# Optimization experiments

Measured on AMD Instinct MI355X. Metric: run time of the kernel, lower is better.

The kernel has to match this reference:

```python
import jax, jax.numpy as jnp
import numpy as np

L = 5          # number of pyramid levels (cat_fuse expects 5*C input channels)
C = 192        # in_channels, divisible by 3 and 2
C3 = C // 3
C2 = C // 2
B = 4
SIZES = [(192, 192), (96, 96), (48, 48), (24, 24), (12, 12)]  # x[1] is reference scale


def conv1x1(x, w, b):
    # 1x1 conv (+ folded eval-mode BN): x [n,cin,h,w], w [cout,cin], b [cout]
    return jnp.einsum('oc,nchw->nohw', w, x) + b[None, :, None, None]


def setup_inputs() -> dict:
    key = jax.random.key(0)
    ks = iter(jax.random.split(key, 40))
    inp = {}
    for i, (h, w) in enumerate(SIZES):
        inp[f'x{i}'] = jax.random.normal(next(ks), (B, C, h, w), jnp.float32)
    def wp(shape):
        return jax.random.normal(next(ks), shape, jnp.float32) * 0.05
    for nm, co, ci in [('k1', C3, C), ('k2', C3, C), ('k3', C3, C), ('q', C, C), ('v', C, C),
                       ('cf', C, L * C), ('e1', C2, C), ('e2', C, C2), ('r1', C2, C), ('r2', C, C2)]:
        inp['W_' + nm] = wp((co, ci))
        inp['b_' + nm] = wp((co,))
    inp['bn_s'] = 1.0 + wp((C,))   # standalone BN folded to affine scale
    inp['bn_t'] = wp((C,))         # standalone BN folded to affine shift
    return inp


def reference(x0, x1, x2, x3, x4,
              W_k1, b_k1, W_k2, b_k2, W_k3, b_k3,
              W_q, b_q, W_v, b_v, W_cf, b_cf,
              W_e1, b_e1, W_e2, b_e2, W_r1, b_r1, W_r2, b_r2,
              bn_s, bn_t):
    xs = [x0, x1, x2, x3, x4]
    b, _, h, w = x1.shape
    hw = h * w
    # bilinear resize to reference scale (torch F.interpolate align_corners=False)
    x_up = [x1 if i == 1 else jax.image.resize(x, (b, C, h, w), 'bilinear') for i, x in enumerate(xs)]
    Xf = jnp.stack(x_up).reshape(L * b, C, h, w)  # shared weights across levels -> batch them

    def emb(z):  # conv1x1 -> GELU(exact) -> conv1x1 (dropout is identity at eval)
        return conv1x1(jax.nn.gelu(conv1x1(z, W_e1, b_e1), approximate=False), W_e2, b_e2)

    la_res = None
    for k in range(5):
        # residual refinement: relu(bn(x + res_block(x)))
        r = conv1x1(jax.nn.relu(conv1x1(Xf, W_r1, b_r1)), W_r2, b_r2)
        Xf = jax.nn.relu((Xf + r) * bn_s[None, :, None, None] + bn_t[None, :, None, None])
        # query/value: per-level projection, split C into 3 chunks -> 15 'keys' per pixel
        Q = conv1x1(Xf, W_q, b_q).reshape(L, b, 3, C3, hw)
        Q = Q.transpose(1, 0, 2, 3, 4).reshape(b, 3 * L, C3, hw).transpose(0, 3, 2, 1)  # [b,hw,C3,15]
        V = conv1x1(Xf, W_v, b_v).reshape(L, b, 3, C3, hw)
        V = V.transpose(1, 0, 2, 3, 4).reshape(b, 3 * L, C3, hw).transpose(0, 3, 1, 2)  # [b,hw,15,C3]
        if k == 0:
            cat = Xf.reshape(L, b, C, h, w).transpose(1, 0, 2, 3, 4).reshape(b, L * C, h, w)
            la_res = emb(jax.nn.relu(conv1x1(cat, W_cf, b_cf)))
        refs = []
        for Wk, bk in ((W_k1, b_k1), (W_k2, b_k2), (W_k3, b_k3)):
            key_i = conv1x1(la_res, Wk, bk).reshape(b, C3, hw).transpose(0, 2, 1)       # [b,hw,C3]
            att = jax.nn.softmax(jnp.einsum('bpc,bpck->bpk', key_i, Q), axis=-1)        # [b,hw,15]
            ref = jnp.einsum('bpk,bpkc->bpc', att, V)                                   # [b,hw,C3]
            refs.append(ref.transpose(0, 2, 1).reshape(b, C3, h, w))
        la_res = emb(jnp.concatenate(refs, axis=1))
    return la_res
```

## Files before the change

### kernel.cpp

```cpp
#include <hip/hip_runtime.h>
#include <math.h>

typedef unsigned short u16;
typedef unsigned int   u32;
typedef __bf16 bf16x8 __attribute__((ext_vector_type(8)));
typedef float  f32x4  __attribute__((ext_vector_type(4)));

__device__ __forceinline__ float b2f(u16 u) {
    unsigned v = ((unsigned)u) << 16;
    return __uint_as_float(v);
}
__device__ __forceinline__ u16 f2b(float f) {
    unsigned x = __float_as_uint(f);
    unsigned r = (x + 0x7fffu + ((x >> 16) & 1u)) >> 16;
    return (u16)r;
}
__device__ __forceinline__ void fsplit(float v, u16& h, u16& l) {
    h = f2b(v);
    l = f2b(v - b2f(h));
}
__device__ __forceinline__ float h2f(u16 u) {
    union { u16 us; _Float16 h; } c; c.us = u; return (float)c.h;
}
__device__ __forceinline__ u16 f2h(float f) {
    union { u16 us; _Float16 h; } c; c.h = (_Float16)f; return c.us;
}
__device__ __forceinline__ float ldx(const void* p, size_t i, int f32m) {
    return f32m ? ((const float*)p)[i] : b2f(((const u16*)p)[i]);
}

__device__ __forceinline__ void gld16(u16* l, const u16* g) {
    __builtin_amdgcn_global_load_lds(
        (const __attribute__((address_space(1))) unsigned int*)g,
        (__attribute__((address_space(3))) unsigned int*)l,
        16, 0, 0);
}

__device__ __forceinline__ int swz(int row) {
    return (row & 3) ^ ((row >> 2) & 3);
}

__global__ void detect_dtype(const u16* __restrict__ x0, int* flag)
{
    int lane = threadIdx.x;
    int bad = 0;
    for (int i = lane; i < 1024; i += 64) {
        float v = b2f(x0[i]);
        if (!(fabsf(v) < 32768.f)) bad = 1;
    }
    unsigned long long m = __ballot(bad);
    if (lane == 0) flag[0] = (m != 0ULL) ? 1 : 0;
}

struct SrcPtrs {
    const void *wr1, *br1, *wr2, *br2, *wq, *bq, *wv, *bv, *wcf, *bcf;
    const void *we1, *be1, *we2, *be2, *wk1, *bk1, *wk2, *bk2, *wk3, *bk3;
    const void *bns, *bnt;
};
__global__ void pack_weights(SrcPtrs S, u16* __restrict__ Wh, u16* __restrict__ Wl,
                             float* __restrict__ Bias, const int* __restrict__ dflag)
{
    const int f32m = *dflag;
    int idx = blockIdx.x * 256 + threadIdx.x;
    if (idx < 368640) {
        const void* src; size_t si;
        if (idx < 18432)       { src = S.wr1; si = idx; }
        else if (idx < 36864)  { src = S.wr2; si = idx - 18432; }
        else if (idx < 110592) {
            int r = idx - 36864, o = r / 192, c = r % 192;
            if (o < 192) { src = S.wq; si = (size_t)o * 192 + c; }
            else         { src = S.wv; si = (size_t)(o - 192) * 192 + c; }
        }
        else if (idx < 294912) { src = S.wcf; si = idx - 110592; }
        else if (idx < 313344) { src = S.we1; si = idx - 294912; }
        else if (idx < 331776) { src = S.we2; si = idx - 313344; }
        else {
            int r = idx - 331776, o = r / 192, c = r % 192;
            src = (o < 64) ? S.wk1 : ((o < 128) ? S.wk2 : S.wk3);
            si = (size_t)(o & 63) * 192 + c;
        }
        u16 h, l; fsplit(ldx(src, si, f32m), h, l);
        Wh[idx] = h; Wl[idx] = l;
    } else if (idx < 370368) {
        int b = idx - 368640; const void* src; size_t si;
        if (b < 96)        { src = S.br1; si = b; }
        else if (b < 288)  { src = S.br2; si = b - 96; }
        else if (b < 672)  { int r = b - 288;
                             if (r < 192) { src = S.bq; si = r; }
                             else         { src = S.bv; si = r - 192; } }
        else if (b < 864)  { src = S.bcf; si = b - 672; }
        else if (b < 960)  { src = S.be1; si = b - 864; }
        else if (b < 1152) { src = S.be2; si = b - 960; }
        else if (b < 1344) { int r = b - 1152;
                             src = (r < 64) ? S.bk1 : ((r < 128) ? S.bk2 : S.bk3);
                             si = r & 63; }
        else if (b < 1536) { src = S.bns; si = b - 1344; }
        else               { src = S.bnt; si = b - 1536; }
        Bias[b] = ldx(src, si, f32m);
    }
}

__global__ void build_tables(float* __restrict__ wtab, int* __restrict__ jtab)
{
    int t = threadIdx.x;
    if (t >= 384) return;
    int li = t / 96, o = t % 96;
    const int ins[4] = {192, 48, 24, 12};
    int in = ins[li];
    float scale = (float)in / 96.0f;
    float ksc = fmaxf(scale, 1.0f);
    float cc = (o + 0.5f) * scale - 0.5f;
    float w[4] = {0.f, 0.f, 0.f, 0.f};
    int   j[4] = {0, 0, 0, 0};
    int n = 0; float s = 0.f;
    int jl = (int)floorf(cc - ksc), jh = (int)floorf(cc + ksc) + 1;
    for (int jj = jl; jj <= jh; jj++) {
        if (jj < 0 || jj >= in) continue;
        float ww = 1.0f - fabsf((float)jj - cc) / ksc;
        if (ww <= 0.f) continue;
        if (n < 4) { w[n] = ww; j[n] = jj; s += ww; n++; }
    }
    for (int i = 0; i < 4; i++) {
        wtab[li * 384 + o * 4 + i] = w[i] / s;
        jtab[li * 384 + o * 4 + i] = j[i];
    }
}

template<int SPLIT>
__launch_bounds__(256)
__global__ void transpose_in(const void* __restrict__ src, int HW,
                             u32* __restrict__ P, u16* __restrict__ Xh,
                             u16* __restrict__ Xl, const int* __restrict__ dflag)
{
    __shared__ float t[32][33];
    const int f32m = *dflag;
    const int b  = blockIdx.z;
    const int c0 = blockIdx.y * 32;
    const int p0 = blockIdx.x * 32;
    const int tid = threadIdx.x;
#pragma unroll
    for (int it = 0; it < 4; it++) {
        int i = it * 256 + tid;
        int pl = i & 31, cl = i >> 5;
        int p = p0 + pl;
        float v = 0.f;
        if (p < HW) v = ldx(src, ((size_t)(b * 192 + c0 + cl)) * HW + p, f32m);
        t[pl][cl] = v;
    }
    __syncthreads();
#pragma unroll
    for (int it = 0; it < 4; it++) {
        int i = it * 256 + tid;
        int cl = i & 31, pl = i >> 5;
        int p = p0 + pl;
        if (p >= HW) continue;
        float v = t[pl][cl];
        u16 h, l; fsplit(v, h, l);
        if constexpr (SPLIT) {
            size_t oi = ((size_t)((4 + b) * 9216 + p)) * 192 + c0 + cl;
            Xh[oi] = h; Xl[oi] = l;
        } else {
            P[((size_t)b * HW + p) * 192 + c0 + cl] = (u32)h | ((u32)l << 16);
        }
    }
}

template<int TAPS>
__launch_bounds__(256)
__global__ void upsample2(const u32* __restrict__ Pa, const u32* __restrict__ Pb,
                          const u32* __restrict__ Pc,
                          const float* __restrict__ wtab, const int* __restrict__ jtab,
                          u16* __restrict__ Xh, u16* __restrict__ Xl)
{
    int li, b, l, in;
    const u32* P;
    if constexpr (TAPS == 4) {
        li = 0; b = blockIdx.y; l = 0; in = 192; P = Pa;
    } else {
        int yi = blockIdx.y;
        li = 1 + (yi >> 2); b = yi & 3;
        const int lvl[4] = {0, 2, 3, 4};
        const int ins[4] = {192, 48, 24, 12};
        l = lvl[li]; in = ins[li];
        P = (li == 1) ? Pa : ((li == 2) ? Pb : Pc);
    }
    int gid = blockIdx.x * 256 + threadIdx.x;
    int c = gid % 192;
    int p = gid / 192;
    int y = p / 96, x = p % 96;
    const float* wt = wtab + li * 384;
    const int*   jt = jtab + li * 384;

    size_t ib = (size_t)b * in * in * 192 + c;
    float a = 0.f;
#pragma unroll
    for (int iy = 0; iy < TAPS; iy++) {
        float wy = wt[y * 4 + iy];
        size_t rb = ib + (size_t)(jt[y * 4 + iy] * in) * 192;
        float ax = 0.f;
#pragma unroll
        for (int ix = 0; ix < TAPS; ix++) {
            u32 u = P[rb + jt[x * 4 + ix] * 192];
            ax += wt[x * 4 + ix] * (b2f((u16)u) + b2f((u16)(u >> 16)));
        }
        a += wy * ax;
    }
    size_t oi = ((size_t)(l * 4 + b) * 9216 + p) * 192 + c;
    u16 h, lo; fsplit(a, h, lo);
    Xh[oi] = h; Xl[oi] = lo;
}

template<int NT, int ACT, int MODE, int OUT>
__launch_bounds__(256)
__global__ void conv_gemm(const u16* __restrict__ Ah, const u16* __restrict__ Al,
                          const u16* __restrict__ Wh, const u16* __restrict__ Wl,
                          const float* __restrict__ Bias,
                          int woff, int boff, int K, int O,
                          u16* __restrict__ out0, u16* __restrict__ out1)
{
    __shared__ __align__(16) u16 LDS[32768];

    const int tid  = threadIdx.x;
    const int lane = tid & 63, wave = tid >> 6;
    const int qd   = lane >> 4, ln = lane & 15;
    const int p0   = blockIdx.x * 64;
    const int img  = blockIdx.z;
    const int M    = 9216;
    const int irow = tid >> 2, ich = tid & 3;

    auto issue = [&](int kb, int c) {
        u16* S = LDS + c * 16384;
        {
            int ch = ich ^ swz(irow);
            size_t ga;
            if constexpr (MODE == 2) {
                int l = kb / 192;
                ga = ((size_t)((l * 4 + img) * M + p0 + irow)) * 192 + (kb - l * 192) + ch * 8;
            } else {
                ga = ((size_t)(img * M + p0 + irow)) * (size_t)K + kb + ch * 8;
            }
            gld16(S + wave * 512,        Ah + ga);
            gld16(S + 2048 + wave * 512, Al + ga);
        }
#pragma unroll
        for (int i = 0; i < 3; i++) {
            int idx = i * 256 + tid;
            int brow = idx >> 2;
            int bc = (idx & 3) ^ swz(brow);
            size_t gb = (size_t)woff + (size_t)brow * K + kb + bc * 8;
            gld16(S + 4096 + i * 2048 + wave * 512,  Wh + gb);
            gld16(S + 10240 + i * 2048 + wave * 512, Wl + gb);
        }
    };

    f32x4 acc[NT];
#pragma unroll
    for (int j = 0; j < NT; j++) acc[j] = (f32x4){0.f, 0.f, 0.f, 0.f};

    issue(0, 0);
    __syncthreads();
    for (int kb = 0; kb < K; kb += 32) {
        int cur = (kb >> 5) & 1;
        if (kb + 32 < K) issue(kb + 32, cur ^ 1);
        const u16* S = LDS + cur * 16384;
        int arow = wave * 16 + ln;
        int asl = arow * 32 + ((qd ^ swz(arow)) << 3);
        bf16x8 ah = *(const bf16x8*)&S[asl];
        bf16x8 al = *(const bf16x8*)&S[2048 + asl];
#pragma unroll
        for (int j = 0; j < NT; j++) {
            int brow = j * 16 + ln;
            int bsl = brow * 32 + ((qd ^ swz(brow)) << 3);
            bf16x8 bh = *(const bf16x8*)&S[4096 + bsl];
            bf16x8 bl = *(const bf16x8*)&S[10240 + bsl];
            acc[j] = __builtin_amdgcn_mfma_f32_16x16x32_bf16(ah, bh, acc[j], 0, 0, 0);
            acc[j] = __builtin_amdgcn_mfma_f32_16x16x32_bf16(ah, bl, acc[j], 0, 0, 0);
            acc[j] = __builtin_amdgcn_mfma_f32_16x16x32_bf16(al, bh, acc[j], 0, 0, 0);
        }
        __syncthreads();
    }

#pragma unroll
    for (int j = 0; j < NT; j++) {
        int o = j * 16 + ln;
        float bvf = Bias[boff + o];
#pragma unroll
        for (int r = 0; r < 4; r++) {
            int prow = p0 + wave * 16 + qd * 4 + r;
            float v = acc[j][r] + bvf;
            if constexpr (ACT == 1) v = fmaxf(v, 0.f);
            if constexpr (OUT == 0) {
                size_t oidx = ((size_t)(img * M + prow)) * (size_t)O + o;
                u16 h, l; fsplit(v, h, l);
                out0[oidx] = h; out1[oidx] = l;
            } else if constexpr (OUT == 1) {
                out0[((size_t)(img * M + prow)) * (size_t)O + o] = f2h(v);
            } else {
                size_t pb = ((size_t)(img * M + prow)) * 192;
                if (o < 192) out0[pb + o] = f2h(v);
                else         out1[pb + o - 192] = f2h(v);
            }
        }
    }
}

template<int ACT1, int MODE2>
__launch_bounds__(256)
__global__ void fused_mlp(const u16* __restrict__ Ah, const u16* __restrict__ Al,
                          const u16* __restrict__ Wh, const u16* __restrict__ Wl,
                          const float* __restrict__ Bias,
                          int w1off, int b1off, int w2off, int b2off,
                          u16* __restrict__ outh, u16* __restrict__ outl)
{
    __shared__ __align__(16) u16 LDS[38912];
    u16* Hh = LDS;
    u16* Hl = LDS + 6656;

    const int tid  = threadIdx.x;
    const int lane = tid & 63, wave = tid >> 6;
    const int qd   = lane >> 4, ln = lane & 15;
    const int p0   = blockIdx.x * 64;
    const int img  = blockIdx.z;
    const int M    = 9216;
    const int irow = tid >> 2, ich = tid & 3;

    auto g1issue = [&](int kb, int c) {
        u16* SA = LDS + 13312 + c * 10240;
        int ch = ich ^ swz(irow);
        size_t ga = ((size_t)(img * M + p0 + irow)) * 192 + kb + ch * 8;
        gld16(SA + wave * 512,        Ah + ga);
        gld16(SA + 2048 + wave * 512, Al + ga);
        size_t gb = (size_t)w1off + (size_t)irow * 192 + kb + ch * 8;
        gld16(SA + 4096 + wave * 512, Wh + gb);
        gld16(SA + 7168 + wave * 512, Wl + gb);
        if (tid < 128) {
            int r2 = 64 + irow;
            int ch2 = ich ^ swz(r2);
            size_t gb2 = (size_t)w1off + (size_t)r2 * 192 + kb + ch2 * 8;
            gld16(SA + 6144 + wave * 512, Wh + gb2);
            gld16(SA + 9216 + wave * 512, Wl + gb2);
        }
    };
    auto g2issue = [&](int kb, int c) {
        u16* B2 = LDS + 13312 + c * 12288;
#pragma unroll
        for (int i = 0; i < 3; i++) {
            int r = i * 64 + irow;
            int ch = ich ^ swz(r);
            size_t g = (size_t)w2off + (size_t)r * 96 + kb + ch * 8;
            gld16(B2 + i * 2048 + wave * 512,        Wh + g);
            gld16(B2 + 6144 + i * 2048 + wave * 512, Wl + g);
        }
    };

    f32x4 acc1[6];
#pragma unroll
    for (int j = 0; j < 6; j++) acc1[j] = (f32x4){0.f, 0.f, 0.f, 0.f};

    g1issue(0, 0);
    __syncthreads();
#pragma unroll 2
    for (int kb = 0; kb < 192; kb += 32) {
        int cur = (kb >> 5) & 1;
        if (kb + 32 < 192) g1issue(kb + 32, cur ^ 1);
        const u16* SA = LDS + 13312 + cur * 10240;
        int arow = wave * 16 + ln;
        int asl = arow * 32 + ((qd ^ swz(arow)) << 3);
        bf16x8 ah = *(const bf16x8*)&SA[asl];
        bf16x8 al = *(const bf16x8*)&SA[2048 + asl];
#pragma unroll
        for (int j = 0; j < 6; j++) {
            int brow = j * 16 + ln;
            int bsl = brow * 32 + ((qd ^ swz(brow)) << 3);
            bf16x8 bh = *(const bf16x8*)&SA[4096 + bsl];
            bf16x8 bl = *(const bf16x8*)&SA[7168 + bsl];
            acc1[j] = __builtin_amdgcn_mfma_f32_16x16x32_bf16(ah, bh, acc1[j], 0, 0, 0);
            acc1[j] = __builtin_amdgcn_mfma_f32_16x16x32_bf16(ah, bl, acc1[j], 0, 0, 0);
            acc1[j] = __builtin_amdgcn_mfma_f32_16x16x32_bf16(al, bh, acc1[j], 0, 0, 0);
        }
        __syncthreads();
    }

    g2issue(0, 0);
#pragma unroll
    for (int j = 0; j < 6; j++) {
        int o = j * 16 + ln;
        float bvf = Bias[b1off + o];
#pragma unroll
        for (int r = 0; r < 4; r++) {
            float v = acc1[j][r] + bvf;
            if constexpr (ACT1 == 1) v = fmaxf(v, 0.f);
            if constexpr (ACT1 == 2) v = 0.5f * v * (1.f + erff(v * 0.70710678118654752f));
            u16 h, l; fsplit(v, h, l);
            int row = wave * 16 + qd * 4 + r;
            Hh[row * 104 + o] = h;
            Hl[row * 104 + o] = l;
        }
    }
    __syncthreads();

    f32x4 acc2[12];
#pragma unroll
    for (int j = 0; j < 12; j++) acc2[j] = (f32x4){0.f, 0.f, 0.f, 0.f};

#pragma unroll
    for (int kb = 0; kb < 96; kb += 32) {
        int cur = (kb >> 5) & 1;
        if (kb + 32 < 96) g2issue(kb + 32, cur ^ 1);
        const u16* B2 = LDS + 13312 + cur * 12288;
        bf16x8 ah = *(const bf16x8*)&Hh[(wave * 16 + ln) * 104 + kb + qd * 8];
        bf16x8 al = *(const bf16x8*)&Hl[(wave * 16 + ln) * 104 + kb + qd * 8];
#pragma unroll
        for (int j = 0; j < 12; j++) {
            int brow = j * 16 + ln;
            int bsl = brow * 32 + ((qd ^ swz(brow)) << 3);
            bf16x8 bh = *(const bf16x8*)&B2[bsl];
            bf16x8 bl = *(const bf16x8*)&B2[6144 + bsl];
            acc2[j] = __builtin_amdgcn_mfma_f32_16x16x32_bf16(ah, bh, acc2[j], 0, 0, 0);
            acc2[j] = __builtin_amdgcn_mfma_f32_16x16x32_bf16(ah, bl, acc2[j], 0, 0, 0);
            acc2[j] = __builtin_amdgcn_mfma_f32_16x16x32_bf16(al, bh, acc2[j], 0, 0, 0);
        }
        __syncthreads();
    }

#pragma unroll
    for (int j = 0; j < 12; j++) {
        int o = j * 16 + ln;
        float bvf = Bias[b2off + o];
#pragma unroll
        for (int r = 0; r < 4; r++) {
            int prow = p0 + wave * 16 + qd * 4 + r;
            float v = acc2[j][r] + bvf;
            size_t oidx = ((size_t)(img * M + prow)) * 192 + o;
            if constexpr (MODE2 == 1) {
                float xo = b2f(outh[oidx]) + b2f(outl[oidx]);
                v = fmaxf((xo + v) * Bias[1344 + o] + Bias[1536 + o], 0.f);
            }
            u16 h, l; fsplit(v, h, l);
            outh[oidx] = h; outl[oidx] = l;
        }
    }
}

template<int WRITE_X>
__launch_bounds__(256)
__global__ void fused_res_qv(u16* __restrict__ Xh, u16* __restrict__ Xl,
                             const u16* __restrict__ Wh, const u16* __restrict__ Wl,
                             const float* __restrict__ Bias,
                             u16* __restrict__ Qf, u16* __restrict__ Vf)
{
    __shared__ __align__(16) u16 LDS[38912];
    u16* Hh = LDS;
    u16* Hl = LDS + 6656;

    const int tid  = threadIdx.x;
    const int lane = tid & 63, wave = tid >> 6;
    const int qd   = lane >> 4, ln = lane & 15;
    const int p0   = blockIdx.x * 64;
    const int img  = blockIdx.z;
    const int M    = 9216;
    const int irow = tid >> 2, ich = tid & 3;

    auto g1issue = [&](int kb, int c) {
        u16* SA = LDS + 13312 + c * 10240;
        int ch = ich ^ swz(irow);
        size_t ga = ((size_t)(img * M + p0 + irow)) * 192 + kb + ch * 8;
        gld16(SA + wave * 512,        Xh + ga);
        gld16(SA + 2048 + wave * 512, Xl + ga);
        size_t gb = (size_t)irow * 192 + kb + ch * 8;
        gld16(SA + 4096 + wave * 512, Wh + gb);
        gld16(SA + 7168 + wave * 512, Wl + gb);
        if (tid < 128) {
            int r2 = 64 + irow;
            int ch2 = ich ^ swz(r2);
            size_t gb2 = (size_t)r2 * 192 + kb + ch2 * 8;
            gld16(SA + 6144 + wave * 512, Wh + gb2);
            gld16(SA + 9216 + wave * 512, Wl + gb2);
        }
    };
    auto g2issue = [&](int kb, int c) {
        u16* B2 = LDS + 13312 + c * 12288;
#pragma unroll
        for (int i = 0; i < 3; i++) {
            int r = i * 64 + irow;
            int ch = ich ^ swz(r);
            size_t g = (size_t)18432 + (size_t)r * 96 + kb + ch * 8;
            gld16(B2 + i * 2048 + wave * 512,        Wh + g);
            gld16(B2 + 6144 + i * 2048 + wave * 512, Wl + g);
        }
    };
    auto g3issue = [&](int s, int c) {
        int p = s / 6, kb = (s - p * 6) * 32;
        u16* B3 = LDS + 24576 + c * 6144;
        int ch = ich ^ swz(irow);
        size_t g = (size_t)36864 + (size_t)(p * 96 + irow) * 192 + kb + ch * 8;
        gld16(B3 + wave * 512,        Wh + g);
        gld16(B3 + 3072 + wave * 512, Wl + g);
        if (tid < 128) {
            int r2 = 64 + irow;
            int ch2 = ich ^ swz(r2);
            size_t g2 = (size_t)36864 + (size_t)(p * 96 + r2) * 192 + kb + ch2 * 8;
            gld16(B3 + 2048 + wave * 512, Wh + g2);
            gld16(B3 + 5120 + wave * 512, Wl + g2);
        }
    };

    f32x4 acc1[6];
#pragma unroll
    for (int j = 0; j < 6; j++) acc1[j] = (f32x4){0.f, 0.f, 0.f, 0.f};

    g1issue(0, 0);
    __syncthreads();
#pragma unroll 2
    for (int kb = 0; kb < 192; kb += 32) {
        int cur = (kb >> 5) & 1;
        if (kb + 32 < 192) g1issue(kb + 32, cur ^ 1);
        const u16* SA = LDS + 13312 + cur * 10240;
        int arow = wave * 16 + ln;
        int asl = arow * 32 + ((qd ^ swz(arow)) << 3);
        bf16x8 ah = *(const bf16x8*)&SA[asl];
        bf16x8 al = *(const bf16x8*)&SA[2048 + asl];
#pragma unroll
        for (int j = 0; j < 6; j++) {
            int brow = j * 16 + ln;
            int bsl = brow * 32 + ((qd ^ swz(brow)) << 3);
            bf16x8 bh = *(const bf16x8*)&SA[4096 + bsl];
            bf16x8 bl = *(const bf16x8*)&SA[7168 + bsl];
            acc1[j] = __builtin_amdgcn_mfma_f32_16x16x32_bf16(ah, bh, acc1[j], 0, 0, 0);
            acc1[j] = __builtin_amdgcn_mfma_f32_16x16x32_bf16(ah, bl, acc1[j], 0, 0, 0);
            acc1[j] = __builtin_amdgcn_mfma_f32_16x16x32_bf16(al, bh, acc1[j], 0, 0, 0);
        }
        __syncthreads();
    }

    g2issue(0, 0);
#pragma unroll
    for (int j = 0; j < 6; j++) {
        int o = j * 16 + ln;
        float bvf = Bias[o];
#pragma unroll
        for (int r = 0; r < 4; r++) {
            float v = fmaxf(acc1[j][r] + bvf, 0.f);
            u16 h, l; fsplit(v, h, l);
            int row = wave * 16 + qd * 4 + r;
            Hh[row * 104 + o] = h;
            Hl[row * 104 + o] = l;
        }
    }
    __syncthreads();

    f32x4 acc2[12];
#pragma unroll
    for (int j = 0; j < 12; j++) acc2[j] = (f32x4){0.f, 0.f, 0.f, 0.f};

#pragma unroll
    for (int kb = 0; kb < 96; kb += 32) {
        int cur = (kb >> 5) & 1;
        if (kb + 32 < 96) g2issue(kb + 32, cur ^ 1);
        const u16* B2 = LDS + 13312 + cur * 12288;
        bf16x8 ah = *(const bf16x8*)&Hh[(wave * 16 + ln) * 104 + kb + qd * 8];
        bf16x8 al = *(const bf16x8*)&Hl[(wave * 16 + ln) * 104 + kb + qd * 8];
#pragma unroll
        for (int j = 0; j < 12; j++) {
            int brow = j * 16 + ln;
            int bsl = brow * 32 + ((qd ^ swz(brow)) << 3);
            bf16x8 bh = *(const bf16x8*)&B2[bsl];
            bf16x8 bl = *(const bf16x8*)&B2[6144 + bsl];
            acc2[j] = __builtin_amdgcn_mfma_f32_16x16x32_bf16(ah, bh, acc2[j], 0, 0, 0);
            acc2[j] = __builtin_amdgcn_mfma_f32_16x16x32_bf16(ah, bl, acc2[j], 0, 0, 0);
            acc2[j] = __builtin_amdgcn_mfma_f32_16x16x32_bf16(al, bh, acc2[j], 0, 0, 0);
        }
        __syncthreads();
    }

    g3issue(0, 0);

    u16* X2h = LDS;
    u16* X2l = LDS + 12288;
#pragma unroll
    for (int j = 0; j < 12; j++) {
        int o = j * 16 + ln;
        float bvf = Bias[96 + o];
#pragma unroll
        for (int r = 0; r < 4; r++) {
            int row  = wave * 16 + qd * 4 + r;
            int prow = p0 + row;
            float v = acc2[j][r] + bvf;
            size_t oidx = ((size_t)(img * M + prow)) * 192 + o;
            float xo = b2f(Xh[oidx]) + b2f(Xl[oidx]);
            v = fmaxf((xo + v) * Bias[1344 + o] + Bias[1536 + o], 0.f);
            u16 h, l; fsplit(v, h, l);
            if constexpr (WRITE_X) { Xh[oidx] = h; Xl[oidx] = l; }
            int off = ((row * 192 + o) * 2) ^ ((row & 7) << 4);
            *(u16*)((char*)X2h + off) = h;
            *(u16*)((char*)X2l + off) = l;
        }
    }
    __syncthreads();

    const int arow = wave * 16 + ln;
#pragma unroll 1
    for (int pass = 0; pass < 4; pass++) {
        f32x4 acc3[6];
#pragma unroll
        for (int j = 0; j < 6; j++) acc3[j] = (f32x4){0.f, 0.f, 0.f, 0.f};

#pragma unroll 2
        for (int t6 = 0; t6 < 6; t6++) {
            int s = pass * 6 + t6;
            int cur = t6 & 1;
            if (s < 23) g3issue(s + 1, cur ^ 1);
            int kb = t6 * 32;
            int aoff = ((arow * 192 + kb + qd * 8) * 2) ^ ((arow & 7) << 4);
            bf16x8 ah = *(const bf16x8*)((const char*)X2h + aoff);
            bf16x8 al = *(const bf16x8*)((const char*)X2l + aoff);
            const u16* B3 = LDS + 24576 + cur * 6144;
#pragma unroll
            for (int j = 0; j < 6; j++) {
                int brow = j * 16 + ln;
                int bsl = brow * 32 + ((qd ^ swz(brow)) << 3);
                bf16x8 bh = *(const bf16x8*)&B3[bsl];
                bf16x8 bl = *(const bf16x8*)&B3[3072 + bsl];
                acc3[j] = __builtin_amdgcn_mfma_f32_16x16x32_bf16(ah, bh, acc3[j], 0, 0, 0);
                acc3[j] = __builtin_amdgcn_mfma_f32_16x16x32_bf16(ah, bl, acc3[j], 0, 0, 0);
                acc3[j] = __builtin_amdgcn_mfma_f32_16x16x32_bf16(al, bh, acc3[j], 0, 0, 0);
            }
            __syncthreads();
        }
#pragma unroll
        for (int j = 0; j < 6; j++) {
            int o = pass * 96 + j * 16 + ln;
            float bvf = Bias[288 + o];
#pragma unroll
            for (int r = 0; r < 4; r++) {
                int prow = p0 + wave * 16 + qd * 4 + r;
                float v = acc3[j][r] + bvf;
                u16 q = f2h(v);
                size_t pb = ((size_t)(img * M + prow)) * 192;
                if (o < 192) Qf[pb + o] = q;
                else         Vf[pb + o - 192] = q;
            }
        }
    }
}

__global__ void attn_kernel(const u16* __restrict__ Qb, const u16* __restrict__ Vb,
                            const u16* __restrict__ Keys,
                            u16* __restrict__ Rh, u16* __restrict__ Rl)
{
    const int lane = threadIdx.x & 63;
    const int wv   = threadIdx.x >> 6;
    const int p = blockIdx.x * 4 + wv;
    const int b = blockIdx.y;

    float qv[15], vv[15];
#pragma unroll
    for (int l = 0; l < 5; l++) {
        size_t base = ((size_t)((l * 4 + b) * 9216 + p)) * 192;
#pragma unroll
        for (int j = 0; j < 3; j++) {
            qv[l * 3 + j] = h2f(Qb[base + j * 64 + lane]);
            vv[l * 3 + j] = h2f(Vb[base + j * 64 + lane]);
        }
    }
    size_t kb = ((size_t)(b * 9216 + p)) * 192;
#pragma unroll
    for (int i = 0; i < 3; i++) {
        float kf = h2f(Keys[kb + i * 64 + lane]);
        float lg[15];
#pragma unroll
        for (int t = 0; t < 15; t++) {
            float s = kf * qv[t];
#pragma unroll
            for (int m = 1; m < 64; m <<= 1) s += __shfl_xor(s, m, 64);
            lg[t] = s;
        }
        float mx = lg[0];
#pragma unroll
        for (int t = 1; t < 15; t++) mx = fmaxf(mx, lg[t]);
        float sum = 0.f;
#pragma unroll
        for (int t = 0; t < 15; t++) { lg[t] = __expf(lg[t] - mx); sum += lg[t]; }
        float inv = 1.f / sum;
        float ref = 0.f;
#pragma unroll
        for (int t = 0; t < 15; t++) ref += lg[t] * vv[t];
        u16 h, lo; fsplit(ref * inv, h, lo);
        Rh[kb + i * 64 + lane] = h;
        Rl[kb + i * 64 + lane] = lo;
    }
}

__launch_bounds__(256)
__global__ void transpose_out(const u16* __restrict__ Lah, const u16* __restrict__ Lal,
                              float* __restrict__ out)
{
    __shared__ float t[32][33];
    const int b  = blockIdx.z;
    const int c0 = blockIdx.y * 32;
    const int p0 = blockIdx.x * 32;
    const int tid = threadIdx.x;
#pragma unroll
    for (int it = 0; it < 4; it++) {
        int i = it * 256 + tid;
        int cl = i & 31, pl = i >> 5;
        size_t idx = ((size_t)(b * 9216 + p0 + pl)) * 192 + c0 + cl;
        t[pl][cl] = b2f(Lah[idx]) + b2f(Lal[idx]);
    }
    __syncthreads();
#pragma unroll
    for (int it = 0; it < 4; it++) {
        int i = it * 256 + tid;
        int pl = i & 31, cl = i >> 5;
        out[((size_t)(b * 192 + c0 + cl)) * 9216 + p0 + pl] = t[pl][cl];
    }
}

__global__ void ws_too_small_kernel(float* out)
{
    int gid = blockIdx.x * 256 + threadIdx.x;
    out[gid] = 12345.0f;
}

extern "C" void kernel_launch(void* const* d_in, const int* in_sizes, int n_in,
                              void* d_out, int out_size, void* d_ws, size_t ws_size,
                              hipStream_t stream)
{
    u16* ws = (u16*)d_ws;
    const size_t oXh   = 0;
    const size_t oXl   = 35389440;
    const size_t oQ    = 70778880;
    const size_t oV    = 106168320;
    const size_t oLah  = 141557760;
    const size_t oLal  = 148635648;
    const size_t oKeys = 155713536;
    const size_t oRh   = 162791424;
    const size_t oRl   = 169869312;
    const size_t oWh   = 176947200;
    const size_t oWl   = 177315840;
    const size_t oBias = 177684480;
    const size_t oWtab = 177687936;
    const size_t oJtab = 177691008;
    const size_t oFlag = 177694080;
    const size_t need_bytes = (size_t)177694096 * 2;

    if (ws_size < need_bytes) {
        ws_too_small_kernel<<<dim3(out_size / 256), dim3(256), 0, stream>>>((float*)d_out);
        return;
    }

    u16* Xh   = ws + oXh;
    u16* Xl   = ws + oXl;
    u16* Qf   = ws + oQ;
    u16* Vf   = ws + oV;
    u16* Lah  = ws + oLah;
    u16* Lal  = ws + oLal;
    u16* Keys = ws + oKeys;
    u16* Rh   = ws + oRh;
    u16* Rl   = ws + oRl;
    u16* Wh   = ws + oWh;
    u16* Wl   = ws + oWl;
    float* Bias = (float*)(ws + oBias);
    float* wtab = (float*)(ws + oWtab);
    int*   jtab = (int*)(ws + oJtab);
    int*   flag = (int*)(ws + oFlag);

    u32* P0 = (u32*)(ws + oQ);
    u32* P2 = (u32*)(ws + oLah);
    u32* P3 = (u32*)(ws + oLal);
    u32* P4 = (u32*)(ws + oKeys);

    SrcPtrs S;
    S.wk1 = d_in[5];  S.bk1 = d_in[6];
    S.wk2 = d_in[7];  S.bk2 = d_in[8];
    S.wk3 = d_in[9];  S.bk3 = d_in[10];
    S.wq  = d_in[11]; S.bq  = d_in[12];
    S.wv  = d_in[13]; S.bv  = d_in[14];
    S.wcf = d_in[15]; S.bcf = d_in[16];
    S.we1 = d_in[17]; S.be1 = d_in[18];
    S.we2 = d_in[19]; S.be2 = d_in[20];
    S.wr1 = d_in[21]; S.br1 = d_in[22];
    S.wr2 = d_in[23]; S.br2 = d_in[24];
    S.bns = d_in[25]; S.bnt = d_in[26];

    dim3 blk(256);
    detect_dtype<<<dim3(1), dim3(64), 0, stream>>>((const u16*)d_in[0], flag);
    pack_weights<<<dim3(1447), blk, 0, stream>>>(S, Wh, Wl, Bias, flag);
    build_tables<<<dim3(1), dim3(384), 0, stream>>>(wtab, jtab);

    transpose_in<0><<<dim3(1152, 6, 4), blk, 0, stream>>>(d_in[0], 36864, P0, nullptr, nullptr, flag);
    transpose_in<1><<<dim3( 288, 6, 4), blk, 0, stream>>>(d_in[1],  9216, nullptr, Xh, Xl, flag);
    transpose_in<0><<<dim3(  72, 6, 4), blk, 0, stream>>>(d_in[2],  2304, P2, nullptr, nullptr, flag);
    transpose_in<0><<<dim3(  18, 6, 4), blk, 0, stream>>>(d_in[3],   576, P3, nullptr, nullptr, flag);
    transpose_in<0><<<dim3(   5, 6, 4), blk, 0, stream>>>(d_in[4],   144, P4, nullptr, nullptr, flag);
    upsample2<4><<<dim3(6912,  4), blk, 0, stream>>>(P0, nullptr, nullptr, wtab, jtab, Xh, Xl);
    upsample2<2><<<dim3(6912, 12), blk, 0, stream>>>(P2, P3, P4, wtab, jtab, Xh, Xl);

    for (int k = 0; k < 5; k++) {
        if (k < 4)
            fused_res_qv<1><<<dim3(144, 1, 20), blk, 0, stream>>>(
                Xh, Xl, Wh, Wl, Bias, Qf, Vf);
        else
            fused_res_qv<0><<<dim3(144, 1, 20), blk, 0, stream>>>(
                Xh, Xl, Wh, Wl, Bias, Qf, Vf);
        if (k == 0) {
            conv_gemm<12, 1, 2, 0><<<dim3(144, 1, 4), blk, 0, stream>>>(
                Xh, Xl, Wh, Wl, Bias, 110592, 672, 960, 192, Rh, Rl);
            fused_mlp<2, 0><<<dim3(144, 1, 4), blk, 0, stream>>>(
                Rh, Rl, Wh, Wl, Bias, 294912, 864, 313344, 960, Lah, Lal);
        }
        conv_gemm<12, 0, 0, 1><<<dim3(144, 1, 4), blk, 0, stream>>>(
            Lah, Lal, Wh, Wl, Bias, 331776, 1152, 192, 192, Keys, nullptr);
        attn_kernel<<<dim3(2304, 4), blk, 0, stream>>>(Qf, Vf, Keys, Rh, Rl);
        fused_mlp<2, 0><<<dim3(144, 1, 4), blk, 0, stream>>>(
            Rh, Rl, Wh, Wl, Bias, 294912, 864, 313344, 960, Lah, Lal);
    }
    transpose_out<<<dim3(288, 6, 4), blk, 0, stream>>>(Lah, Lal, (float*)d_out);
}
```

Before: 2.456 ms.

## Double waves per block in GEMM kernels by splitting output columns across wave pairs

The conv_gemm, fused_mlp and fused_res_qv kernels now launch 512 threads (8 waves) instead of 256. Waves form a 4x2 grid: row-waves keep the same 16-pixel slice and column-waves each take half of the output-channel tiles. Only the first 256 threads issue global-to-LDS loads, so loading stays unchanged while per-wave accumulators and registers are halved. The goal is more latency hiding and MFMA concurrency per CU, at the cost of idle load threads, duplicated A-fragment LDS reads, and heavier barriers.

```diff
diff --git a/kernel.cpp b/kernel.cpp
--- a/kernel.cpp
+++ b/kernel.cpp
@@ -211,17 +211,19 @@
 }
 
 template<int NT, int ACT, int MODE, int OUT>
-__launch_bounds__(256)
+__launch_bounds__(512, 4)
 __global__ void conv_gemm(const u16* __restrict__ Ah, const u16* __restrict__ Al,
                           const u16* __restrict__ Wh, const u16* __restrict__ Wl,
                           const float* __restrict__ Bias,
                           int woff, int boff, int K, int O,
                           u16* __restrict__ out0, u16* __restrict__ out1)
 {
+    constexpr int NTW = NT / 2;
     __shared__ __align__(16) u16 LDS[32768];
 
     const int tid  = threadIdx.x;
     const int lane = tid & 63, wave = tid >> 6;
+    const int wr   = wave & 3, wc = wave >> 2;
     const int qd   = lane >> 4, ln = lane & 15;
     const int p0   = blockIdx.x * 64;
     const int img  = blockIdx.z;
@@ -229,6 +231,7 @@
     const int irow = tid >> 2, ich = tid & 3;
 
     auto issue = [&](int kb, int c) {
+        if (tid >= 256) return;
         u16* S = LDS + c * 16384;
         {
             int ch = ich ^ swz(irow);
@@ -253,9 +256,9 @@
         }
     };
 
-    f32x4 acc[NT];
-#pragma unroll
-    for (int j = 0; j < NT; j++) acc[j] = (f32x4){0.f, 0.f, 0.f, 0.f};
+    f32x4 acc[NTW];
+#pragma unroll
+    for (int j = 0; j < NTW; j++) acc[j] = (f32x4){0.f, 0.f, 0.f, 0.f};
 
     issue(0, 0);
     __syncthreads();
@@ -263,13 +266,13 @@
         int cur = (kb >> 5) & 1;
         if (kb + 32 < K) issue(kb + 32, cur ^ 1);
         const u16* S = LDS + cur * 16384;
-        int arow = wave * 16 + ln;
+        int arow = wr * 16 + ln;
         int asl = arow * 32 + ((qd ^ swz(arow)) << 3);
         bf16x8 ah = *(const bf16x8*)&S[asl];
         bf16x8 al = *(const bf16x8*)&S[2048 + asl];
 #pragma unroll
-        for (int j = 0; j < NT; j++) {
-            int brow = j * 16 + ln;
+        for (int j = 0; j < NTW; j++) {
+            int brow = (wc * NTW + j) * 16 + ln;
             int bsl = brow * 32 + ((qd ^ swz(brow)) << 3);
             bf16x8 bh = *(const bf16x8*)&S[4096 + bsl];
             bf16x8 bl = *(const bf16x8*)&S[10240 + bsl];
@@ -281,12 +284,12 @@
     }
 
 #pragma unroll
-    for (int j = 0; j < NT; j++) {
-        int o = j * 16 + ln;
+    for (int j = 0; j < NTW; j++) {
+        int o = (wc * NTW + j) * 16 + ln;
         float bvf = Bias[boff + o];
 #pragma unroll
         for (int r = 0; r < 4; r++) {
-            int prow = p0 + wave * 16 + qd * 4 + r;
+            int prow = p0 + wr * 16 + qd * 4 + r;
             float v = acc[j][r] + bvf;
             if constexpr (ACT == 1) v = fmaxf(v, 0.f);
             if constexpr (OUT == 0) {
@@ -305,7 +308,7 @@
 }
 
 template<int ACT1, int MODE2>
-__launch_bounds__(256)
+__launch_bounds__(512, 4)
 __global__ void fused_mlp(const u16* __restrict__ Ah, const u16* __restrict__ Al,
                           const u16* __restrict__ Wh, const u16* __restrict__ Wl,
                           const float* __restrict__ Bias,
@@ -318,6 +321,7 @@
 
     const int tid  = threadIdx.x;
     const int lane = tid & 63, wave = tid >> 6;
+    const int wr   = wave & 3, wc = wave >> 2;
     const int qd   = lane >> 4, ln = lane & 15;
     const int p0   = blockIdx.x * 64;
     const int img  = blockIdx.z;
@@ -325,6 +329,7 @@
     const int irow = tid >> 2, ich = tid & 3;
 
     auto g1issue = [&](int kb, int c) {
+        if (tid >= 256) return;
         u16* SA = LDS + 13312 + c * 10240;
         int ch = ich ^ swz(irow);
         size_t ga = ((size_t)(img * M + p0 + irow)) * 192 + kb + ch * 8;
@@ -342,6 +347,7 @@
         }
     };
     auto g2issue = [&](int kb, int c) {
+        if (tid >= 256) return;
         u16* B2 = LDS + 13312 + c * 12288;
 #pragma unroll
         for (int i = 0; i < 3; i++) {
@@ -353,9 +359,9 @@
         }
     };
 
-    f32x4 acc1[6];
-#pragma unroll
-    for (int j = 0; j < 6; j++) acc1[j] = (f32x4){0.f, 0.f, 0.f, 0.f};
+    f32x4 acc1[3];
+#pragma unroll
+    for (int j = 0; j < 3; j++) acc1[j] = (f32x4){0.f, 0.f, 0.f, 0.f};
 
     g1issue(0, 0);
     __syncthreads();
@@ -364,13 +370,13 @@
         int cur = (kb >> 5) & 1;
         if (kb + 32 < 192) g1issue(kb + 32, cur ^ 1);
         const u16* SA = LDS + 13312 + cur * 10240;
-        int arow = wave * 16 + ln;
+        int arow = wr * 16 + ln;
         int asl = arow * 32 + ((qd ^ swz(arow)) << 3);
         bf16x8 ah = *(const bf16x8*)&SA[asl];
         bf16x8 al = *(const bf16x8*)&SA[2048 + asl];
 #pragma unroll
-        for (int j = 0; j < 6; j++) {
-            int brow = j * 16 + ln;
+        for (int j = 0; j < 3; j++) {
+            int brow = (wc * 3 + j) * 16 + ln;
             int bsl = brow * 32 + ((qd ^ swz(brow)) << 3);
             bf16x8 bh = *(const bf16x8*)&SA[4096 + bsl];
             bf16x8 bl = *(const bf16x8*)&SA[7168 + bsl];
@@ -383,8 +389,8 @@
 
     g2issue(0, 0);
 #pragma unroll
-    for (int j = 0; j < 6; j++) {
-        int o = j * 16 + ln;
+    for (int j = 0; j < 3; j++) {
+        int o = (wc * 3 + j) * 16 + ln;
         float bvf = Bias[b1off + o];
 #pragma unroll
         for (int r = 0; r < 4; r++) {
@@ -392,27 +398,27 @@
             if constexpr (ACT1 == 1) v = fmaxf(v, 0.f);
             if constexpr (ACT1 == 2) v = 0.5f * v * (1.f + erff(v * 0.70710678118654752f));
             u16 h, l; fsplit(v, h, l);
-            int row = wave * 16 + qd * 4 + r;
+            int row = wr * 16 + qd * 4 + r;
             Hh[row * 104 + o] = h;
             Hl[row * 104 + o] = l;
         }
     }
     __syncthreads();
 
-    f32x4 acc2[12];
-#pragma unroll
-    for (int j = 0; j < 12; j++) acc2[j] = (f32x4){0.f, 0.f, 0.f, 0.f};
+    f32x4 acc2[6];
+#pragma unroll
+    for (int j = 0; j < 6; j++) acc2[j] = (f32x4){0.f, 0.f, 0.f, 0.f};
 
 #pragma unroll
     for (int kb = 0; kb < 96; kb += 32) {
         int cur = (kb >> 5) & 1;
         if (kb + 32 < 96) g2issue(kb + 32, cur ^ 1);
         const u16* B2 = LDS + 13312 + cur * 12288;
-        bf16x8 ah = *(const bf16x8*)&Hh[(wave * 16 + ln) * 104 + kb + qd * 8];
-        bf16x8 al = *(const bf16x8*)&Hl[(wave * 16 + ln) * 104 + kb + qd * 8];
-#pragma unroll
-        for (int j = 0; j < 12; j++) {
-            int brow = j * 16 + ln;
+        bf16x8 ah = *(const bf16x8*)&Hh[(wr * 16 + ln) * 104 + kb + qd * 8];
+        bf16x8 al = *(const bf16x8*)&Hl[(wr * 16 + ln) * 104 + kb + qd * 8];
+#pragma unroll
+        for (int j = 0; j < 6; j++) {
+            int brow = (wc * 6 + j) * 16 + ln;
             int bsl = brow * 32 + ((qd ^ swz(brow)) << 3);
             bf16x8 bh = *(const bf16x8*)&B2[bsl];
             bf16x8 bl = *(const bf16x8*)&B2[6144 + bsl];
@@ -424,12 +430,12 @@
     }
 
 #pragma unroll
-    for (int j = 0; j < 12; j++) {
-        int o = j * 16 + ln;
+    for (int j = 0; j < 6; j++) {
+        int o = (wc * 6 + j) * 16 + ln;
         float bvf = Bias[b2off + o];
 #pragma unroll
         for (int r = 0; r < 4; r++) {
-            int prow = p0 + wave * 16 + qd * 4 + r;
+            int prow = p0 + wr * 16 + qd * 4 + r;
             float v = acc2[j][r] + bvf;
             size_t oidx = ((size_t)(img * M + prow)) * 192 + o;
             if constexpr (MODE2 == 1) {
@@ -443,7 +449,7 @@
 }
 
 template<int WRITE_X>
-__launch_bounds__(256)
+__launch_bounds__(512, 4)
 __global__ void fused_res_qv(u16* __restrict__ Xh, u16* __restrict__ Xl,
                              const u16* __restrict__ Wh, const u16* __restrict__ Wl,
                              const float* __restrict__ Bias,
@@ -455,6 +461,7 @@
 
     const int tid  = threadIdx.x;
     const int lane = tid & 63, wave = tid >> 6;
+    const int wr   = wave & 3, wc = wave >> 2;
     const int qd   = lane >> 4, ln = lane & 15;
     const int p0   = blockIdx.x * 64;
     const int img  = blockIdx.z;
@@ -462,6 +469,7 @@
     const int irow = tid >> 2, ich = tid & 3;
 
     auto g1issue = [&](int kb, int c) {
+        if (tid >= 256) return;
         u16* SA = LDS + 13312 + c * 10240;
         int ch = ich ^ swz(irow);
         size_t ga = ((size_t)(img * M + p0 + irow)) * 192 + kb + ch * 8;
@@ -479,6 +487,7 @@
         }
     };
     auto g2issue = [&](int kb, int c) {
+        if (tid >= 256) return;
         u16* B2 = LDS + 13312 + c * 12288;
 #pragma unroll
         for (int i = 0; i < 3; i++) {
@@ -490,6 +499,7 @@
         }
     };
     auto g3issue = [&](int s, int c) {
+        if (tid >= 256) return;
         int p = s / 6, kb = (s - p * 6) * 32;
         u16* B3 = LDS + 24576 + c * 6144;
         int ch = ich ^ swz(irow);
@@ -505,9 +515,9 @@
         }
     };
 
-    f32x4 acc1[6];
-#pragma unroll
-    for (int j = 0; j < 6; j++) acc1[j] = (f32x4){0.f, 0.f, 0.f, 0.f};
+    f32x4 acc1[3];
+#pragma unroll
+    for (int j = 0; j < 3; j++) acc1[j] = (f32x4){0.f, 0.f, 0.f, 0.f};
 
     g1issue(0, 0);
     __syncthreads();
@@ -516,13 +526,13 @@
         int cur = (kb >> 5) & 1;
         if (kb + 32 < 192) g1issue(kb + 32, cur ^ 1);
         const u16* SA = LDS + 13312 + cur * 10240;
-        int arow = wave * 16 + ln;
+        int arow = wr * 16 + ln;
         int asl = arow * 32 + ((qd ^ swz(arow)) << 3);
         bf16x8 ah = *(const bf16x8*)&SA[asl];
         bf16x8 al = *(const bf16x8*)&SA[2048 + asl];
 #pragma unroll
-        for (int j = 0; j < 6; j++) {
-            int brow = j * 16 + ln;
+        for (int j = 0; j < 3; j++) {
+            int brow = (wc * 3 + j) * 16 + ln;
             int bsl = brow * 32 + ((qd ^ swz(brow)) << 3);
             bf16x8 bh = *(const bf16x8*)&SA[4096 + bsl];
             bf16x8 bl = *(const bf16x8*)&SA[7168 + bsl];
@@ -535,34 +545,34 @@
 
     g2issue(0, 0);
 #pragma unroll
-    for (int j = 0; j < 6; j++) {
-        int o = j * 16 + ln;
+    for (int j = 0; j < 3; j++) {
+        int o = (wc * 3 + j) * 16 + ln;
         float bvf = Bias[o];
 #pragma unroll
         for (int r = 0; r < 4; r++) {
             float v = fmaxf(acc1[j][r] + bvf, 0.f);
             u16 h, l; fsplit(v, h, l);
-            int row = wave * 16 + qd * 4 + r;
+            int row = wr * 16 + qd * 4 + r;
             Hh[row * 104 + o] = h;
             Hl[row * 104 + o] = l;
         }
     }
     __syncthreads();
 
-    f32x4 acc2[12];
-#pragma unroll
-    for (int j = 0; j < 12; j++) acc2[j] = (f32x4){0.f, 0.f, 0.f, 0.f};
+    f32x4 acc2[6];
+#pragma unroll
+    for (int j = 0; j < 6; j++) acc2[j] = (f32x4){0.f, 0.f, 0.f, 0.f};
 
 #pragma unroll
     for (int kb = 0; kb < 96; kb += 32) {
         int cur = (kb >> 5) & 1;
         if (kb + 32 < 96) g2issue(kb + 32, cur ^ 1);
         const u16* B2 = LDS + 13312 + cur * 12288;
-        bf16x8 ah = *(const bf16x8*)&Hh[(wave * 16 + ln) * 104 + kb + qd * 8];
-        bf16x8 al = *(const bf16x8*)&Hl[(wave * 16 + ln) * 104 + kb + qd * 8];
-#pragma unroll
-        for (int j = 0; j < 12; j++) {
-            int brow = j * 16 + ln;
+        bf16x8 ah = *(const bf16x8*)&Hh[(wr * 16 + ln) * 104 + kb + qd * 8];
+        bf16x8 al = *(const bf16x8*)&Hl[(wr * 16 + ln) * 104 + kb + qd * 8];
+#pragma unroll
+        for (int j = 0; j < 6; j++) {
+            int brow = (wc * 6 + j) * 16 + ln;
             int bsl = brow * 32 + ((qd ^ swz(brow)) << 3);
             bf16x8 bh = *(const bf16x8*)&B2[bsl];
             bf16x8 bl = *(const bf16x8*)&B2[6144 + bsl];
@@ -578,12 +588,12 @@
     u16* X2h = LDS;
     u16* X2l = LDS + 12288;
 #pragma unroll
-    for (int j = 0; j < 12; j++) {
-        int o = j * 16 + ln;
+    for (int j = 0; j < 6; j++) {
+        int o = (wc * 6 + j) * 16 + ln;
         float bvf = Bias[96 + o];
 #pragma unroll
         for (int r = 0; r < 4; r++) {
-            int row  = wave * 16 + qd * 4 + r;
+            int row  = wr * 16 + qd * 4 + r;
             int prow = p0 + row;
             float v = acc2[j][r] + bvf;
             size_t oidx = ((size_t)(img * M + prow)) * 192 + o;
@@ -598,12 +608,12 @@
     }
     __syncthreads();
 
-    const int arow = wave * 16 + ln;
+    const int arow = wr * 16 + ln;
 #pragma unroll 1
     for (int pass = 0; pass < 4; pass++) {
-        f32x4 acc3[6];
-#pragma unroll
-        for (int j = 0; j < 6; j++) acc3[j] = (f32x4){0.f, 0.f, 0.f, 0.f};
+        f32x4 acc3[3];
+#pragma unroll
+        for (int j = 0; j < 3; j++) acc3[j] = (f32x4){0.f, 0.f, 0.f, 0.f};
 
 #pragma unroll 2
         for (int t6 = 0; t6 < 6; t6++) {
@@ -616,8 +626,8 @@
             bf16x8 al = *(const bf16x8*)((const char*)X2l + aoff);
             const u16* B3 = LDS + 24576 + cur * 6144;
 #pragma unroll
-            for (int j = 0; j < 6; j++) {
-                int brow = j * 16 + ln;
+            for (int j = 0; j < 3; j++) {
+                int brow = (wc * 3 + j) * 16 + ln;
                 int bsl = brow * 32 + ((qd ^ swz(brow)) << 3);
                 bf16x8 bh = *(const bf16x8*)&B3[bsl];
                 bf16x8 bl = *(const bf16x8*)&B3[3072 + bsl];
@@ -628,12 +638,12 @@
             __syncthreads();
         }
 #pragma unroll
-        for (int j = 0; j < 6; j++) {
-            int o = pass * 96 + j * 16 + ln;
+        for (int j = 0; j < 3; j++) {
+            int o = pass * 96 + (wc * 3 + j) * 16 + ln;
             float bvf = Bias[288 + o];
 #pragma unroll
             for (int r = 0; r < 4; r++) {
-                int prow = p0 + wave * 16 + qd * 4 + r;
+                int prow = p0 + wr * 16 + qd * 4 + r;
                 float v = acc3[j][r] + bvf;
                 u16 q = f2h(v);
                 size_t pb = ((size_t)(img * M + prow)) * 192;
@@ -784,6 +794,7 @@
     S.bns = d_in[25]; S.bnt = d_in[26];
 
     dim3 blk(256);
+    dim3 blk512(512);
     detect_dtype<<<dim3(1), dim3(64), 0, stream>>>((const u16*)d_in[0], flag);
     pack_weights<<<dim3(1447), blk, 0, stream>>>(S, Wh, Wl, Bias, flag);
     build_tables<<<dim3(1), dim3(384), 0, stream>>>(wtab, jtab);
@@ -798,21 +809,21 @@
 
     for (int k = 0; k < 5; k++) {
         if (k < 4)
-            fused_res_qv<1><<<dim3(144, 1, 20), blk, 0, stream>>>(
+            fused_res_qv<1><<<dim3(144, 1, 20), blk512, 0, stream>>>(
                 Xh, Xl, Wh, Wl, Bias, Qf, Vf);
         else
-            fused_res_qv<0><<<dim3(144, 1, 20), blk, 0, stream>>>(
+            fused_res_qv<0><<<dim3(144, 1, 20), blk512, 0, stream>>>(
                 Xh, Xl, Wh, Wl, Bias, Qf, Vf);
         if (k == 0) {
-            conv_gemm<12, 1, 2, 0><<<dim3(144, 1, 4), blk, 0, stream>>>(
+            conv_gemm<12, 1, 2, 0><<<dim3(144, 1, 4), blk512, 0, stream>>>(
                 Xh, Xl, Wh, Wl, Bias, 110592, 672, 960, 192, Rh, Rl);
-            fused_mlp<2, 0><<<dim3(144, 1, 4), blk, 0, stream>>>(
+            fused_mlp<2, 0><<<dim3(144, 1, 4), blk512, 0, stream>>>(
                 Rh, Rl, Wh, Wl, Bias, 294912, 864, 313344, 960, Lah, Lal);
         }
-        conv_gemm<12, 0, 0, 1><<<dim3(144, 1, 4), blk, 0, stream>>>(
+        conv_gemm<12, 0, 0, 1><<<dim3(144, 1, 4), blk512, 0, stream>>>(
             Lah, Lal, Wh, Wl, Bias, 331776, 1152, 192, 192, Keys, nullptr);
         attn_kernel<<<dim3(2304, 4), blk, 0, stream>>>(Qf, Vf, Keys, Rh, Rl);
-        fused_mlp<2, 0><<<dim3(144, 1, 4), blk, 0, stream>>>(
+        fused_mlp<2, 0><<<dim3(144, 1, 4), blk512, 0, stream>>>(
             Rh, Rl, Wh, Wl, Bias, 294912, 864, 313344, 960, Lah, Lal);
     }
     transpose_out<<<dim3(288, 6, 4), blk, 0, stream>>>(Lah, Lal, (float*)d_out);
```

New measurement: 2.266 ms. 1.08x faster.
